# Performance work log

Measured on AMD Instinct MI355X. Metric: run time of the kernel, lower is better.

The kernel has to match this reference:

```python
import jax, jax.numpy as jnp
import numpy as np

N = 256          # fft_size == len(root_sequence)
B = 8            # batch
S = 14           # num_ofdm_symbols
PILOTS = [0, 7]  # pilot OFDM symbol indices
U = 1            # ZC root index


def _gather_index_list():
    # pilot symbols -> 0 (reference shift), data symbols -> 1..num_data
    out, k = [], 1
    for s in range(S):
        if s in PILOTS:
            out.append(0)
        else:
            out.append(k)
            k += 1
    return np.asarray(out, dtype=np.int32)


def setup_inputs() -> dict:
    key = jax.random.key(0)
    ks = jax.random.split(key, 5)
    # Zadoff-Chu root sequence (unit modulus) -> real/imag float32 parts
    n = np.arange(N, dtype=np.float64)
    zc = np.exp(-1j * np.pi * U * n * (n + 1) / N)
    return {
        "x_real": jax.random.normal(ks[0], (B, S, N), dtype=jnp.float32),
        "x_imag": jax.random.normal(ks[1], (B, S, N), dtype=jnp.float32),
        "cov_real": jax.random.normal(ks[2], (N, N, N), dtype=jnp.float32) * 0.05,
        "cov_imag": jax.random.normal(ks[3], (N, N, N), dtype=jnp.float32) * 0.05,
        "zc_real": jnp.asarray(zc.real, dtype=jnp.float32),
        "zc_imag": jnp.asarray(zc.imag, dtype=jnp.float32),
        "shift_val": jax.random.randint(ks[4], (B, S - len(PILOTS)), 0, N, dtype=jnp.int32),
        "gather_idx": jnp.asarray(_gather_index_list()),
    }


def reference(x_real, x_imag, cov_real, cov_imag, zc_real, zc_imag, shift_val, gather_idx):
    x = (x_real + 1j * x_imag).astype(jnp.complex64)            # [B, S, N] received symbols
    cov = (cov_real + 1j * cov_imag).astype(jnp.complex64)      # [N, N, N] LMMSE covariance blocks
    zc = (zc_real + 1j * zc_imag).astype(jnp.complex64)         # [N] root sequence

    # complete_shift_val: prepend reference shift (0), remap via gather_index_list
    complete = jnp.pad(shift_val, ((0, 0), (1, 0)), constant_values=0)  # [B, 1+num_data]
    complete = complete[:, gather_idx]                                   # [B, S]

    # ifft_zc0 = sionna (orthonormal) ifft of the root sequence, shape [1,1,N]
    ifft_zc0 = jnp.fft.ifft(zc, norm="ortho").astype(jnp.complex64)[None, None, :]

    # FFT-based normalized circular cross-correlation along the last axis
    cc = jnp.fft.ifft(jnp.fft.fft(x, axis=-1) * jnp.conj(jnp.fft.fft(ifft_zc0, axis=-1)), axis=-1)
    h_time_est = (cc / jnp.sqrt(jnp.float32(N))).astype(jnp.complex64)   # [B, S, N]

    h_freq_est = jnp.fft.fft(h_time_est, axis=-1).astype(jnp.complex64)  # [B, S, N]

    # LMMSE_TrueP: gather per-shift [N,N] covariance block, apply as mat-vec
    block = cov[complete]                                                # [B, S, N, N]
    h_freq_est = jnp.einsum("bsnm,bsm->bsn", block, h_freq_est)          # [B, S, N]
    return h_freq_est
```

## Files before the change

kernel.cpp:

```cpp
#include <hip/hip_runtime.h>
#include <math.h>

static constexpr int kN   = 256;
static constexpr int kB   = 8;
static constexpr int kS   = 14;
static constexpr int kNSH = 12;
static constexpr int kBS  = kB * kS;

__global__ __launch_bounds__(256) void dft_zc_kernel(
    const float* __restrict__ xr, const float* __restrict__ xi,
    const float* __restrict__ zcr, const float* __restrict__ zci,
    float* __restrict__ hre, float* __restrict__ him)
{
    __shared__ float sxr[kN];
    __shared__ float sxi[kN];
    const int bs = blockIdx.x;
    const int k  = threadIdx.x;

    sxr[k] = xr[bs * kN + k];
    sxi[k] = xi[bs * kN + k];

    const float two_pi_over_N = 6.283185307179586476925f / (float)kN;
    float wi, wr;
    sincosf(-two_pi_over_N * (float)k, &wi, &wr);

    __syncthreads();

    float Hr = 0.0f, Hi = 0.0f;

    for (int n0 = 0; n0 < kN; n0 += 32) {
        const int p = (k * n0) & (kN - 1);
        float ci, cr;
        sincosf(-two_pi_over_N * (float)p, &ci, &cr);
        #pragma unroll
        for (int j = 0; j < 32; ++j) {
            const int n = n0 + j;
            const float a = sxr[n];
            const float b = sxi[n];
            Hr = fmaf(a, cr, fmaf(-b, ci, Hr));
            Hi = fmaf(a, ci, fmaf( b, cr, Hi));
            const float nr = cr * wr - ci * wi;
            const float ni = cr * wi + ci * wr;
            cr = nr; ci = ni;
        }
    }

    const float zr = zcr[k], zi = zci[k];
    hre[bs * kN + k] = fmaf(Hr, zr,  Hi * zi);
    him[bs * kN + k] = fmaf(Hi, zr, -Hr * zi);
}

__global__ __launch_bounds__(256) void matvec_kernel(
    const float* __restrict__ covr, const float* __restrict__ covi,
    const float* __restrict__ hre, const float* __restrict__ him,
    const int*  __restrict__ shift, const int* __restrict__ gidx,
    float* __restrict__ out)
{
    const int bs = blockIdx.x >> 3;
    const int o  = blockIdx.x & 7;
    const int s  = bs % kS;
    const int b  = bs / kS;

    const int g = gidx[s];
    const int c = (g == 0) ? 0 : shift[b * kNSH + (g - 1)];

    const int tid = threadIdx.x;
    const int w   = tid >> 6;
    const int l   = tid & 63;

    const float4 hr = ((const float4*)(hre + bs * kN))[l];
    const float4 hi = ((const float4*)(him + bs * kN))[l];

    const long base = (long)c * (long)(kN * kN);
    const float* __restrict__ rb = covr + base;
    const float* __restrict__ ib = covi + base;
    const int n0 = o * 32 + w * 8;

    float4 mr[8], mi[8];
    #pragma unroll
    for (int r = 0; r < 8; ++r) {
        mr[r] = ((const float4*)(rb + (long)(n0 + r) * kN))[l];
        mi[r] = ((const float4*)(ib + (long)(n0 + r) * kN))[l];
    }

    float ar[8], ai[8];
    #pragma unroll
    for (int r = 0; r < 8; ++r) {
        ar[r] = mr[r].x*hr.x + mr[r].y*hr.y + mr[r].z*hr.z + mr[r].w*hr.w
              - (mi[r].x*hi.x + mi[r].y*hi.y + mi[r].z*hi.z + mi[r].w*hi.w);
        ai[r] = mr[r].x*hi.x + mr[r].y*hi.y + mr[r].z*hi.z + mr[r].w*hi.w
              +  mi[r].x*hr.x + mi[r].y*hr.y + mi[r].z*hr.z + mi[r].w*hr.w;
    }

    #pragma unroll
    for (int off = 32; off > 0; off >>= 1) {
        #pragma unroll
        for (int r = 0; r < 8; ++r) {
            ar[r] += __shfl_xor(ar[r], off, 64);
            ai[r] += __shfl_xor(ai[r], off, 64);
        }
    }

    if (l == 0) {
        #pragma unroll
        for (int r = 0; r < 8; ++r) {
            out[(long)bs * kN + n0 + r]                    = ar[r];
            out[(long)(kBS * kN) + (long)bs * kN + n0 + r] = ai[r];
        }
    }
}

extern "C" void kernel_launch(void* const* d_in, const int* in_sizes, int n_in,
                              void* d_out, int out_size, void* d_ws, size_t ws_size,
                              hipStream_t stream) {
    const float* xr    = (const float*)d_in[0];
    const float* xi    = (const float*)d_in[1];
    const float* covr  = (const float*)d_in[2];
    const float* covi  = (const float*)d_in[3];
    const float* zcr   = (const float*)d_in[4];
    const float* zci   = (const float*)d_in[5];
    const int*   shift = (const int*)d_in[6];
    const int*   gidx  = (const int*)d_in[7];

    float* hre = (float*)d_ws;
    float* him = hre + kBS * kN;

    dft_zc_kernel<<<kBS, 256, 0, stream>>>(xr, xi, zcr, zci, hre, him);
    matvec_kernel<<<kBS * 8, 256, 0, stream>>>(covr, covi, hre, him, shift, gidx,
                                               (float*)d_out);
}
```

Measured before the change: 147.7 us.

## Split DFT into partial sums across blocks and fold reduction into matvec

The DFT stage is split so each 64-thread block computes a quarter of the input contributions for 64 output bins. That turns 112 blocks into 1792 and shortens each thread's serial loop by a factor of four. Partial sums go to workspace, and the matvec kernel sums the four partials and applies the ZC conjugate multiply before the covariance mat-vec. The matvec also moves to 64-thread blocks with four times as many blocks. The cost is extra workspace traffic and each matvec block redundantly reducing the partials.

```diff
diff --git a/kernel.cpp b/kernel.cpp
--- a/kernel.cpp
+++ b/kernel.cpp
@@ -7,18 +7,23 @@
 static constexpr int kNSH = 12;
 static constexpr int kBS  = kB * kS;
 
-__global__ __launch_bounds__(256) void dft_zc_kernel(
+static constexpr int kWsPlane = 4 * kBS * kN;
+
+__global__ __launch_bounds__(64) void dft_part_kernel(
     const float* __restrict__ xr, const float* __restrict__ xi,
-    const float* __restrict__ zcr, const float* __restrict__ zci,
-    float* __restrict__ hre, float* __restrict__ him)
+    float* __restrict__ wsR, float* __restrict__ wsI)
 {
-    __shared__ float sxr[kN];
-    __shared__ float sxi[kN];
-    const int bs = blockIdx.x;
-    const int k  = threadIdx.x;
+    __shared__ float sxr[64];
+    __shared__ float sxi[64];
+    const int blk = blockIdx.x;
+    const int bs  = blk >> 4;
+    const int q   = (blk >> 2) & 3;
+    const int kg  = blk & 3;
+    const int l   = threadIdx.x;
+    const int k   = kg * 64 + l;
 
-    sxr[k] = xr[bs * kN + k];
-    sxi[k] = xi[bs * kN + k];
+    sxr[l] = xr[bs * kN + q * 64 + l];
+    sxi[l] = xi[bs * kN + q * 64 + l];
 
     const float two_pi_over_N = 6.283185307179586476925f / (float)kN;
     float wi, wr;
@@ -28,15 +33,16 @@
 
     float Hr = 0.0f, Hi = 0.0f;
 
-    for (int n0 = 0; n0 < kN; n0 += 32) {
-        const int p = (k * n0) & (kN - 1);
+    #pragma unroll
+    for (int c = 0; c < 2; ++c) {
+        const int n0 = q * 64 + c * 32;
+        const int p  = (k * n0) & (kN - 1);
         float ci, cr;
         sincosf(-two_pi_over_N * (float)p, &ci, &cr);
         #pragma unroll
         for (int j = 0; j < 32; ++j) {
-            const int n = n0 + j;
-            const float a = sxr[n];
-            const float b = sxi[n];
+            const float a = sxr[c * 32 + j];
+            const float b = sxi[c * 32 + j];
             Hr = fmaf(a, cr, fmaf(-b, ci, Hr));
             Hi = fmaf(a, ci, fmaf( b, cr, Hi));
             const float nr = cr * wr - ci * wi;
@@ -45,43 +51,54 @@
         }
     }
 
-    const float zr = zcr[k], zi = zci[k];
-    hre[bs * kN + k] = fmaf(Hr, zr,  Hi * zi);
-    him[bs * kN + k] = fmaf(Hi, zr, -Hr * zi);
+    wsR[(q * kBS + bs) * kN + k] = Hr;
+    wsI[(q * kBS + bs) * kN + k] = Hi;
 }
 
-__global__ __launch_bounds__(256) void matvec_kernel(
+__global__ __launch_bounds__(64) void matvec_kernel(
     const float* __restrict__ covr, const float* __restrict__ covi,
-    const float* __restrict__ hre, const float* __restrict__ him,
+    const float* __restrict__ wsR,  const float* __restrict__ wsI,
+    const float* __restrict__ zcr,  const float* __restrict__ zci,
     const int*  __restrict__ shift, const int* __restrict__ gidx,
     float* __restrict__ out)
 {
-    const int bs = blockIdx.x >> 3;
-    const int o  = blockIdx.x & 7;
+    const int bs = blockIdx.x >> 5;
+    const int r0 = (blockIdx.x & 31) * 8;
     const int s  = bs % kS;
     const int b  = bs / kS;
 
     const int g = gidx[s];
     const int c = (g == 0) ? 0 : shift[b * kNSH + (g - 1)];
 
-    const int tid = threadIdx.x;
-    const int w   = tid >> 6;
-    const int l   = tid & 63;
-
-    const float4 hr = ((const float4*)(hre + bs * kN))[l];
-    const float4 hi = ((const float4*)(him + bs * kN))[l];
+    const int l = threadIdx.x;
 
     const long base = (long)c * (long)(kN * kN);
     const float* __restrict__ rb = covr + base;
     const float* __restrict__ ib = covi + base;
-    const int n0 = o * 32 + w * 8;
 
     float4 mr[8], mi[8];
     #pragma unroll
     for (int r = 0; r < 8; ++r) {
-        mr[r] = ((const float4*)(rb + (long)(n0 + r) * kN))[l];
-        mi[r] = ((const float4*)(ib + (long)(n0 + r) * kN))[l];
+        mr[r] = ((const float4*)(rb + (long)(r0 + r) * kN))[l];
+        mi[r] = ((const float4*)(ib + (long)(r0 + r) * kN))[l];
     }
+
+    float4 Hr = make_float4(0.f, 0.f, 0.f, 0.f);
+    float4 Hi = make_float4(0.f, 0.f, 0.f, 0.f);
+    #pragma unroll
+    for (int q = 0; q < 4; ++q) {
+        const float4 pr = ((const float4*)(wsR + (q * kBS + bs) * kN))[l];
+        const float4 pi = ((const float4*)(wsI + (q * kBS + bs) * kN))[l];
+        Hr.x += pr.x; Hr.y += pr.y; Hr.z += pr.z; Hr.w += pr.w;
+        Hi.x += pi.x; Hi.y += pi.y; Hi.z += pi.z; Hi.w += pi.w;
+    }
+    const float4 zr = ((const float4*)zcr)[l];
+    const float4 zi = ((const float4*)zci)[l];
+    float4 hr, hi;
+    hr.x = fmaf(Hr.x, zr.x,  Hi.x * zi.x);  hi.x = fmaf(Hi.x, zr.x, -Hr.x * zi.x);
+    hr.y = fmaf(Hr.y, zr.y,  Hi.y * zi.y);  hi.y = fmaf(Hi.y, zr.y, -Hr.y * zi.y);
+    hr.z = fmaf(Hr.z, zr.z,  Hi.z * zi.z);  hi.z = fmaf(Hi.z, zr.z, -Hr.z * zi.z);
+    hr.w = fmaf(Hr.w, zr.w,  Hi.w * zi.w);  hi.w = fmaf(Hi.w, zr.w, -Hr.w * zi.w);
 
     float ar[8], ai[8];
     #pragma unroll
@@ -104,8 +121,8 @@
     if (l == 0) {
         #pragma unroll
         for (int r = 0; r < 8; ++r) {
-            out[(long)bs * kN + n0 + r]                    = ar[r];
-            out[(long)(kBS * kN) + (long)bs * kN + n0 + r] = ai[r];
+            out[(long)bs * kN + r0 + r]                    = ar[r];
+            out[(long)(kBS * kN) + (long)bs * kN + r0 + r] = ai[r];
         }
     }
 }
@@ -122,10 +139,10 @@
     const int*   shift = (const int*)d_in[6];
     const int*   gidx  = (const int*)d_in[7];
 
-    float* hre = (float*)d_ws;
-    float* him = hre + kBS * kN;
+    float* wsR = (float*)d_ws;
+    float* wsI = wsR + kWsPlane;
 
-    dft_zc_kernel<<<kBS, 256, 0, stream>>>(xr, xi, zcr, zci, hre, him);
-    matvec_kernel<<<kBS * 8, 256, 0, stream>>>(covr, covi, hre, him, shift, gidx,
-                                               (float*)d_out);
+    dft_part_kernel<<<kBS * 16, 64, 0, stream>>>(xr, xi, wsR, wsI);
+    matvec_kernel<<<kBS * 32, 64, 0, stream>>>(covr, covi, wsR, wsI, zcr, zci,
+                                               shift, gidx, (float*)d_out);
 }
```

Result: no change. 145.4 us (-1.6%).
